# Kernel tuning notes

Measured on AMD Instinct MI355X. Metric: run time of the kernel, lower is better.

The kernel has to match this reference:

```python
import jax, jax.numpy as jnp
import numpy as np

B, S, D, Fd, M, H, L = 4, 1024, 1024, 4096, 512, 16, 2
HD = D // H
EPS = 1e-5


def _ln(x, s, b):
    m = jnp.mean(x, axis=-1, keepdims=True)
    v = jnp.mean((x - m) ** 2, axis=-1, keepdims=True)
    return (x - m) * jax.lax.rsqrt(v + EPS) * s + b


def _mha(x, Wq, bq, Wk, bk, Wv, bv, Wo, bo):
    b_, s_, _ = x.shape
    Q = (x @ Wq + bq).reshape(b_, s_, H, HD)
    K = (x @ Wk + bk).reshape(b_, s_, H, HD)
    V = (x @ Wv + bv).reshape(b_, s_, H, HD)
    scores = jnp.einsum('bihd,bjhd->bhij', Q, K) / np.sqrt(HD).astype(np.float32)
    w = jax.nn.softmax(scores, axis=-1)
    out = jnp.einsum('bhij,bjhd->bihd', w, V).reshape(b_, s_, D)
    return out @ Wo + bo


def setup_inputs() -> dict:
    key = jax.random.key(0)
    ks = iter(jax.random.split(key, 40))
    w = lambda shape: jax.random.normal(next(ks), shape, jnp.float32) * 0.02
    inp = {
        'x': jax.random.normal(next(ks), (B, S, D), jnp.float32),
        # stacked per-global-layer params [L, ...]
        'Wq': w((L, D, D)), 'bq': jnp.zeros((L, D)),
        'Wk': w((L, D, D)), 'bk': jnp.zeros((L, D)),
        'Wv': w((L, D, D)), 'bv': jnp.zeros((L, D)),
        'Wo': w((L, D, D)), 'bo': jnp.zeros((L, D)),
        'W1': w((L, D, Fd)), 'b1': jnp.zeros((L, Fd)),
        'W2': w((L, Fd, D)), 'b2': jnp.zeros((L, D)),
        'n1s': jnp.ones((L, D)), 'n1b': jnp.zeros((L, D)),
        'n2s': jnp.ones((L, D)), 'n2b': jnp.zeros((L, D)),
        # top-level params
        'ln1s': jnp.ones((D,)), 'ln1b': jnp.zeros((D,)),
        'ln2s': jnp.ones((D,)), 'ln2b': jnp.zeros((D,)),
        'ln3s': jnp.ones((D,)), 'ln3b': jnp.zeros((D,)),
        'Wb': w((D, M)), 'bb': jnp.zeros((M,)),      # backbone stand-in
        'Wm': w((M, D)), 'bm': jnp.zeros((D,)),      # self.linear
        'Wf1': w((D, Fd)), 'bf1': jnp.zeros((Fd,)),  # top feed_forward
        'Wf2': w((Fd, D)), 'bf2': jnp.zeros((D,)),
    }
    return inp


def reference(x, Wq, bq, Wk, bk, Wv, bv, Wo, bo, W1, b1, W2, b2,
              n1s, n1b, n2s, n2b, ln1s, ln1b, ln2s, ln2b, ln3s, ln3b,
              Wb, bb, Wm, bm, Wf1, bf1, Wf2, bf2):
    # dropout is identity (eval mode)
    # global branch: stacked EncoderLayers
    g = x
    for i in range(L):
        a = _mha(g, Wq[i], bq[i], Wk[i], bk[i], Wv[i], bv[i], Wo[i], bo[i])
        g = _ln(g + a, n1s[i], n1b[i])
        ff = jax.nn.relu(g @ W1[i] + b1[i]) @ W2[i] + b2[i]
        g = _ln(g + ff, n2s[i], n2b[i])

    def local(frac):
        st = S // frac
        xs = x[:, -st:, :]
        mo = (xs @ Wb + bb) @ Wm + bm
        y = _ln(xs + mo, ln1s, ln1b)
        return jnp.pad(y, ((0, 0), (S - st, 0), (0, 0)))

    output = g + local(2) + local(4)  # S >= 4 branch
    h = _ln(output + x, ln2s, ln2b)
    ff = jax.nn.relu(output @ Wf1 + bf1) @ Wf2 + bf2
    return _ln(h + ff, ln3s, ln3b)
```

## Files before the change

### kernel.cpp

```cpp
#include <hip/hip_runtime.h>
#include <stdint.h>


typedef short   s16x8 __attribute__((ext_vector_type(8)));
typedef float   f32x4 __attribute__((ext_vector_type(4)));
typedef uint16_t u16x8 __attribute__((ext_vector_type(8)));
typedef uint16_t u16x4 __attribute__((ext_vector_type(4)));

__device__ __forceinline__ float bf2f(uint16_t h) {
    union { uint32_t u; float f; } c; c.u = ((uint32_t)h) << 16; return c.f;
}
__device__ __forceinline__ uint16_t f2bf(float f) {
    union { float f; uint32_t u; } c; c.f = f;
    uint32_t u = c.u;
    u += 0x7fffu + ((u >> 16) & 1u);
    return (uint16_t)(u >> 16);
}
__device__ __forceinline__ uint32_t cvt_pk_bf16(float lo, float hi) {
    uint32_t r;
    asm("v_cvt_pk_bf16_f32 %0, %1, %2" : "=v"(r) : "v"(lo), "v"(hi));
    return r;
}

__device__ __forceinline__ void g2l16(const uint16_t* g, uint16_t* l) {
    __builtin_amdgcn_global_load_lds(
        (const __attribute__((address_space(1))) void*)g,
        (__attribute__((address_space(3))) void*)l, 16, 0, 0);
}

template<int MODE>
__global__ __launch_bounds__(256, 2) void gemm128n(
    const uint16_t* __restrict__ A, const uint16_t* __restrict__ Bt,
    const float* __restrict__ bias0, const float* __restrict__ bias1,
    const float* __restrict__ bias2,
    uint16_t* __restrict__ C0, uint16_t* __restrict__ C1,
    uint16_t* __restrict__ C2,
    int N)
{
    __shared__ __align__(16) uint16_t smem[36864];
    uint16_t* sA = smem;
    uint16_t* sB = smem + 12288;

    const int t    = threadIdx.x;
    const int w    = t >> 6;
    const int lane = t & 63;
    const int qd   = lane >> 4;
    const int cc   = lane & 15;
    const int wn   = w * 64;

    const int id  = blockIdx.x;
    const int loc = id >> 3;
    const int bm  = (id & 7) * 4 + (loc & 3);
    const int bn  = loc >> 2;
    const int m0  = bm * 128;
    const int n0  = bn * 256;

    const float* bp = bias0;
    int n0c = n0;
    if (MODE == 3) {
        int seg = n0 >> 10;
        n0c = n0 & 1023;
        bp = (seg == 0) ? bias0 : (seg == 1) ? bias1 : bias2;
    }
    float bb[4];
#pragma unroll
    for (int j = 0; j < 4; ++j) bb[j] = bp[n0c + wn + j * 16 + cc];

    int offA[8], offB[4];
#pragma unroll
    for (int i = 0; i < 8; ++i) {
        int ml = i * 16 + cc;
        offA[i] = ml * 32 + ((qd ^ ((ml >> 1) & 3)) * 8);
    }
#pragma unroll
    for (int j = 0; j < 4; ++j) {
        int nl = wn + j * 16 + cc;
        offB[j] = nl * 32 + ((qd ^ ((nl >> 1) & 3)) * 8);
    }

    const uint16_t* pA[2]; int ldA[2];
#pragma unroll
    for (int is = 0; is < 2; ++is) {
        int gc = is * 256 + t;
        int row = gc >> 2, ph = gc & 3;
        pA[is]  = A + (size_t)(m0 + row) * 1024 + (ph ^ ((row >> 1) & 3)) * 8;
        ldA[is] = (is * 256 + w * 64) * 8;
    }
    const uint16_t* pB[4]; int ldB[4];
#pragma unroll
    for (int is = 0; is < 4; ++is) {
        int gc = is * 256 + t;
        int row = gc >> 2, ph = gc & 3;
        pB[is]  = Bt + (size_t)(n0 + row) * 1024 + (ph ^ ((row >> 1) & 3)) * 8;
        ldB[is] = (is * 256 + w * 64) * 8;
    }
    auto stage = [&](int tt, int slot) {
        int kt = tt * 32;
        uint16_t* dA = sA + slot * 4096;
        uint16_t* dB = sB + slot * 8192;
#pragma unroll
        for (int is = 0; is < 2; ++is) g2l16(pA[is] + kt, dA + ldA[is]);
#pragma unroll
        for (int is = 0; is < 4; ++is) g2l16(pB[is] + kt, dB + ldB[is]);
    };

    f32x4 acc[8][4];
#pragma unroll
    for (int i = 0; i < 8; ++i)
#pragma unroll
        for (int j = 0; j < 4; ++j) acc[i][j] = (f32x4)0.0f;

    stage(0, 0); stage(1, 1);
    asm volatile("s_waitcnt vmcnt(6)" ::: "memory");
    __builtin_amdgcn_s_barrier();

    int cur = 0, pf = 2;
#pragma unroll 1
    for (int kt = 0; kt < 32; ++kt) {
        const uint16_t* sa = sA + cur * 4096;
        const uint16_t* sb = sB + cur * 8192;
        s16x8 av[8], bv[4];
#pragma unroll
        for (int j = 0; j < 4; ++j) bv[j] = *(const s16x8*)(sb + offB[j]);
#pragma unroll
        for (int i = 0; i < 8; ++i) av[i] = *(const s16x8*)(sa + offA[i]);
        if (kt < 30) stage(kt + 2, pf);
        asm volatile("s_waitcnt lgkmcnt(0)" ::: "memory");
        __builtin_amdgcn_sched_barrier(0);
        __builtin_amdgcn_s_setprio(1);
#pragma unroll
        for (int i = 0; i < 8; ++i)
#pragma unroll
            for (int j = 0; j < 4; ++j)
                acc[i][j] = __builtin_amdgcn_mfma_f32_16x16x32_bf16(
                    av[i], bv[j], acc[i][j], 0, 0, 0);
        __builtin_amdgcn_s_setprio(0);
        if (kt < 30)       { asm volatile("s_waitcnt vmcnt(6)" ::: "memory"); }
        else if (kt == 30) { asm volatile("s_waitcnt vmcnt(0)" ::: "memory"); }
        __builtin_amdgcn_s_barrier();
        pf = cur;
        cur = (cur == 2) ? 0 : cur + 1;
    }

    if (MODE == 3 && (n0 >> 10) == 2) {
#pragma unroll
        for (int j = 0; j < 4; ++j) {
            int c = n0c + wn + j * 16 + cc;
            int hh = c >> 6, d = c & 63;
#pragma unroll
            for (int i = 0; i < 8; ++i) {
                int rb = m0 + i * 16 + qd * 4;
                int b = rb >> 10, s = rb & 1023;
                u16x4 o;
#pragma unroll
                for (int r = 0; r < 4; ++r) o[r] = f2bf(acc[i][j][r] + bb[j]);
                *(u16x4*)(C2 + ((size_t)((b * 16 + hh) * 64 + d)) * 1024 + s) = o;
            }
        }
        return;
    }
    {
        uint16_t* C = C0;
        int Nc = N;
        if (MODE == 3) {
            int seg = n0 >> 10;
            C = (seg == 0) ? C0 : C1;
            Nc = 1024;
        }
        constexpr int ST = 264;
#pragma unroll
        for (int i = 0; i < 8; ++i)
#pragma unroll
            for (int j = 0; j < 4; ++j) {
                f32x4 v = acc[i][j];
#pragma unroll
                for (int r = 0; r < 4; ++r) {
                    float val = v[r] + bb[j];
                    if (MODE == 1) val = fmaxf(val, 0.0f);
                    smem[(i * 16 + qd * 4 + r) * ST + wn + j * 16 + cc] = f2bf(val);
                }
            }
        __syncthreads();
#pragma unroll
        for (int p = 0; p < 16; ++p) {
            int row  = p * 8 + (t >> 5);
            int colc = (t & 31) * 8;
            u16x8 v = *(const u16x8*)(smem + row * ST + colc);
            *(u16x8*)(C + (size_t)(m0 + row) * Nc + n0c + colc) = v;
        }
    }
}

template<int MODE, int BN, int BK, int DB>
__global__ __launch_bounds__(256) void gemm_bt(
    const uint16_t* __restrict__ A, const uint16_t* __restrict__ Bt,
    const float* __restrict__ bias0, const float* __restrict__ bias1,
    const float* __restrict__ bias2,
    uint16_t* __restrict__ C0, uint16_t* __restrict__ C1,
    uint16_t* __restrict__ C2,
    int M, int N, int K)
{
    constexpr int JN   = BN / 32;
    constexpr int KS   = BK / 32;
    constexpr int CPR  = BK / 8;
    constexpr int LG   = (BK == 32) ? 2 : 3;
    constexpr int RA   = (128 * BK / 8) / 256;
    constexpr int RB   = (BN  * BK / 8) / 256;
    constexpr int NBUF = DB ? 2 : 1;
    constexpr int STG  = NBUF * (128 + BN) * BK;
    constexpr int EPI  = (MODE == 3) ? 0 : 128 * (BN + 8);
    constexpr int SMEM = (STG > EPI) ? STG : EPI;
    __shared__ __align__(16) uint16_t smem[SMEM];
    uint16_t* sAp = smem;
    uint16_t* sBp = smem + NBUF * 128 * BK;

    const int t    = threadIdx.x;
    const int w    = t >> 6;
    const int lane = t & 63;
    const int qd   = lane >> 4;
    const int cc   = lane & 15;

    int bm, bn;
    {
        int gx = gridDim.x, gy = gridDim.y;
        if ((gy & 7) == 0) {
            int id   = blockIdx.y * gx + blockIdx.x;
            int gpg  = gy >> 3;
            int rest = id >> 3;
            bm = (id & 7) * gpg + rest % gpg;
            bn = rest / gpg;
        } else { bm = blockIdx.y; bn = blockIdx.x; }
    }
    const int m0 = bm * 128;
    const int n0 = bn * BN;
    const int wm = (w >> 1) * 64;
    const int wn = (w & 1) * (BN / 2);

    auto key = [](int row) -> int {
        return (BK == 32) ? ((row >> 1) & 3) : (row & 7);
    };

    f32x4 acc[4][JN];
#pragma unroll
    for (int i = 0; i < 4; ++i)
#pragma unroll
        for (int j = 0; j < JN; ++j) acc[i][j] = (f32x4)0.0f;

    int rA[RA], kA[RA];
#pragma unroll
    for (int is = 0; is < RA; ++is) {
        int gc = is * 256 + t;
        int row = gc >> LG, ph = gc & (CPR - 1);
        rA[is] = row;
        kA[is] = (ph ^ key(row)) * 8;
    }
    int rB[RB], kB[RB];
#pragma unroll
    for (int is = 0; is < RB; ++is) {
        int gc = is * 256 + t;
        int row = gc >> LG, ph = gc & (CPR - 1);
        rB[is] = row;
        kB[is] = (ph ^ key(row)) * 8;
    }
    int offA[4][KS], offB[JN][KS];
#pragma unroll
    for (int i = 0; i < 4; ++i) {
        int ml = wm + i * 16 + cc;
#pragma unroll
        for (int ks = 0; ks < KS; ++ks)
            offA[i][ks] = ml * BK + ((ks * 4 + qd) ^ key(ml)) * 8;
    }
#pragma unroll
    for (int j = 0; j < JN; ++j) {
        int nl = wn + j * 16 + cc;
#pragma unroll
        for (int ks = 0; ks < KS; ++ks)
            offB[j][ks] = nl * BK + ((ks * 4 + qd) ^ key(nl)) * 8;
    }

    auto stage = [&](int kt, int buf) {
#pragma unroll
        for (int is = 0; is < RA; ++is)
            g2l16(A + (size_t)(m0 + rA[is]) * K + kt + kA[is],
                  sAp + (size_t)buf * 128 * BK + (size_t)(is * 256 + w * 64) * 8);
#pragma unroll
        for (int is = 0; is < RB; ++is)
            g2l16(Bt + (size_t)(n0 + rB[is]) * K + kt + kB[is],
                  sBp + (size_t)buf * BN * BK + (size_t)(is * 256 + w * 64) * 8);
    };
    auto compute = [&](int buf) {
        const uint16_t* sa = sAp + (size_t)buf * 128 * BK;
        const uint16_t* sb = sBp + (size_t)buf * BN * BK;
#pragma unroll
        for (int ks = 0; ks < KS; ++ks) {
            s16x8 af[4], bv[JN];
#pragma unroll
            for (int i = 0; i < 4; ++i) af[i] = *(const s16x8*)(sa + offA[i][ks]);
#pragma unroll
            for (int j = 0; j < JN; ++j) bv[j] = *(const s16x8*)(sb + offB[j][ks]);
#pragma unroll
            for (int i = 0; i < 4; ++i)
#pragma unroll
                for (int j = 0; j < JN; ++j)
                    acc[i][j] = __builtin_amdgcn_mfma_f32_16x16x32_bf16(
                        af[i], bv[j], acc[i][j], 0, 0, 0);
        }
    };

    if (DB) {
        stage(0, 0);
        __syncthreads();
        int cur = 0;
        for (int kt = 0; kt < K; kt += BK) {
            if (kt + BK < K) stage(kt + BK, cur ^ 1);
            compute(cur);
            __syncthreads();
            cur ^= 1;
        }
    } else {
        for (int kt = 0; kt < K; kt += BK) {
            stage(kt, 0);
            __syncthreads();
            compute(0);
            __syncthreads();
        }
    }

    if (MODE == 3) {
#pragma unroll
        for (int j = 0; j < JN; ++j) {
            int col = n0 + wn + j * 16 + cc;
            int seg = col >> 10;
            const float* bp = (seg == 0) ? bias0 : (seg == 1) ? bias1 : bias2;
            float bb = bp[col & 1023];
#pragma unroll
            for (int i = 0; i < 4; ++i) {
                f32x4 v = acc[i][j];
#pragma unroll
                for (int r = 0; r < 4; ++r) {
                    float val = v[r] + bb;
                    int row = m0 + wm + i * 16 + qd * 4 + r;
                    if (col < 1024) {
                        C0[(size_t)row * 1024 + col] = f2bf(val);
                    } else if (col < 2048) {
                        C1[(size_t)row * 1024 + (col - 1024)] = f2bf(val);
                    } else {
                        int c = col - 2048;
                        int b = row >> 10, s = row & 1023;
                        int hh = c >> 6, d = c & 63;
                        C2[((size_t)(b * 16 + hh) * 64 + d) * 1024 + s] = f2bf(val);
                    }
                }
            }
        }
    } else {
        constexpr int ST = BN + 8;
#pragma unroll
        for (int j = 0; j < JN; ++j) {
            int col = wn + j * 16 + cc;
            float bb = bias0[n0 + col];
#pragma unroll
            for (int i = 0; i < 4; ++i) {
                f32x4 v = acc[i][j];
#pragma unroll
                for (int r = 0; r < 4; ++r) {
                    float val = v[r] + bb;
                    if (MODE == 1) val = fmaxf(val, 0.0f);
                    smem[(wm + i * 16 + qd * 4 + r) * ST + col] = f2bf(val);
                }
            }
        }
        __syncthreads();
        constexpr int NP  = 128 * BN / 2048;
        constexpr int TPR = BN / 8;
#pragma unroll
        for (int p = 0; p < NP; ++p) {
            int row  = p * (256 / TPR) + t / TPR;
            int colc = (t % TPR) * 8;
            u16x8 v = *(const u16x8*)(smem + row * ST + colc);
            *(u16x8*)(C0 + (size_t)(m0 + row) * N + n0 + colc) = v;
        }
    }
}

#define FA_P 76
__global__ __launch_bounds__(256) void flash_attn(
    const uint16_t* __restrict__ Q, const uint16_t* __restrict__ K,
    const uint16_t* __restrict__ Vt, uint16_t* __restrict__ O)
{
    __shared__ __align__(16) uint16_t QPs[64 * FA_P];
    __shared__ __align__(16) uint16_t Ks[64 * FA_P];
    __shared__ __align__(16) uint16_t Vs[64 * FA_P];

    const int t    = threadIdx.x;
    const int w    = t >> 6;
    const int lane = t & 63;
    const int qd   = lane >> 4;
    const int cc   = lane & 15;
    const int id   = blockIdx.x;
    const int xg   = id & 7;
    const int loc  = id >> 3;
    const int bh   = xg * 8 + (loc >> 4);
    const int qblk = loc & 15;
    const int b    = bh >> 4, hh = bh & 15;
    const size_t rowbase = (size_t)b * 1024;

    int rr[2], ch8[2], lws[2];
    const uint16_t* Kp[2];
    const uint16_t* Vp[2];
#pragma unroll
    for (int is = 0; is < 2; ++is) {
        int c   = is * 256 + t;
        rr[is]  = c >> 3;
        ch8[is] = (c & 7) * 8;
        lws[is] = rr[is] * FA_P + ch8[is];
        Kp[is]  = K  + (rowbase + rr[is]) * 1024 + hh * 64 + ch8[is];
        Vp[is]  = Vt + ((size_t)(bh * 64 + rr[is])) * 1024 + ch8[is];
    }

    u16x8 kr[2], vr[2];
#pragma unroll
    for (int is = 0; is < 2; ++is) {
        kr[is] = *(const u16x8*)(Kp[is]);
        vr[is] = *(const u16x8*)(Vp[is]);
    }

#pragma unroll
    for (int is = 0; is < 2; ++is)
        *(u16x8*)(QPs + lws[is]) =
            *(const u16x8*)(Q + (rowbase + qblk * 64 + rr[is]) * 1024 + hh * 64 + ch8[is]);
    __syncthreads();
    s16x8 aq0 = *(const s16x8*)(QPs + (w * 16 + cc) * FA_P + qd * 8);
    s16x8 aq1 = *(const s16x8*)(QPs + (w * 16 + cc) * FA_P + 32 + qd * 8);
    __syncthreads();

    f32x4 o[4];
    float lrow[4] = {0.0f, 0.0f, 0.0f, 0.0f};
#pragma unroll
    for (int j = 0; j < 4; ++j) o[j] = (f32x4)0.0f;

#pragma unroll 1
    for (int kb = 64; kb <= 1024; kb += 64) {
#pragma unroll
        for (int is = 0; is < 2; ++is) {
            *(u16x8*)(Ks + lws[is]) = kr[is];
            *(u16x8*)(Vs + lws[is]) = vr[is];
        }
        if (kb < 1024) {
#pragma unroll
            for (int is = 0; is < 2; ++is) {
                kr[is] = *(const u16x8*)(Kp[is] + (size_t)kb * 1024);
                vr[is] = *(const u16x8*)(Vp[is] + kb);
            }
        }
        __syncthreads();

        f32x4 sc[4];
#pragma unroll
        for (int j = 0; j < 4; ++j) {
            s16x8 b0 = *(const s16x8*)(Ks + (j * 16 + cc) * FA_P + qd * 8);
            s16x8 b1 = *(const s16x8*)(Ks + (j * 16 + cc) * FA_P + 32 + qd * 8);
            sc[j] = __builtin_amdgcn_mfma_f32_16x16x32_bf16(aq0, b0, (f32x4)0.0f, 0, 0, 0);
            sc[j] = __builtin_amdgcn_mfma_f32_16x16x32_bf16(aq1, b1, sc[j], 0, 0, 0);
        }

#pragma unroll
        for (int r = 0; r < 4; ++r) {
            float p0 = __expf(sc[0][r] * 0.125f);
            float p1 = __expf(sc[1][r] * 0.125f);
            float p2 = __expf(sc[2][r] * 0.125f);
            float p3 = __expf(sc[3][r] * 0.125f);
            lrow[r] += (p0 + p1) + (p2 + p3);
            int prow = (w * 16 + qd * 4 + r) * FA_P + cc;
            uint32_t pk01 = cvt_pk_bf16(p0, p1);
            uint32_t pk23 = cvt_pk_bf16(p2, p3);
            QPs[prow]      = (uint16_t)pk01;
            QPs[prow + 16] = (uint16_t)(pk01 >> 16);
            QPs[prow + 32] = (uint16_t)pk23;
            QPs[prow + 48] = (uint16_t)(pk23 >> 16);
        }

#pragma unroll
        for (int ks = 0; ks < 2; ++ks) {
            s16x8 ap = *(const s16x8*)(QPs + (w * 16 + cc) * FA_P + ks * 32 + qd * 8);
#pragma unroll
            for (int j = 0; j < 4; ++j) {
                s16x8 bv = *(const s16x8*)(Vs + (j * 16 + cc) * FA_P + ks * 32 + qd * 8);
                o[j] = __builtin_amdgcn_mfma_f32_16x16x32_bf16(ap, bv, o[j], 0, 0, 0);
            }
        }
        __syncthreads();
    }

#pragma unroll
    for (int r = 0; r < 4; ++r) {
        float rs = lrow[r];
        rs += __shfl_xor(rs, 1);
        rs += __shfl_xor(rs, 2);
        rs += __shfl_xor(rs, 4);
        rs += __shfl_xor(rs, 8);
        float inv = 1.0f / rs;
        size_t grow = rowbase + qblk * 64 + w * 16 + qd * 4 + r;
#pragma unroll
        for (int j = 0; j < 4; ++j)
            O[grow * 1024 + hh * 64 + j * 16 + cc] = f2bf(o[j][r] * inv);
    }
}

template<int BT, int F32OUT>
__global__ __launch_bounds__(256) void ln_res(
    const uint16_t* __restrict__ A, const void* __restrict__ Bp,
    const float* __restrict__ S, const float* __restrict__ Bi,
    void* __restrict__ outp)
{
    const int row = blockIdx.x, t = threadIdx.x;
    const int w = t >> 6, lane = t & 63;
    u16x4 a4 = *(const u16x4*)(A + (size_t)row * 1024 + t * 4);
    float bvals[4];
    if (BT == 0) {
        u16x4 b4 = *(const u16x4*)((const uint16_t*)Bp + (size_t)row * 1024 + t * 4);
#pragma unroll
        for (int e = 0; e < 4; ++e) bvals[e] = bf2f(b4[e]);
    } else {
        float4 b4 = *(const float4*)((const float*)Bp + (size_t)row * 1024 + t * 4);
        bvals[0] = b4.x; bvals[1] = b4.y; bvals[2] = b4.z; bvals[3] = b4.w;
    }
    float v[4], sum = 0.0f, sq = 0.0f;
#pragma unroll
    for (int e = 0; e < 4; ++e) {
        v[e] = bf2f(a4[e]) + bvals[e];
        sum += v[e];
        sq  += v[e] * v[e];
    }
#pragma unroll
    for (int d = 1; d < 64; d <<= 1) {
        sum += __shfl_xor(sum, d);
        sq  += __shfl_xor(sq, d);
    }
    __shared__ float rs[4], rq[4];
    if (lane == 0) { rs[w] = sum; rq[w] = sq; }
    __syncthreads();
    sum = rs[0] + rs[1] + rs[2] + rs[3];
    sq  = rq[0] + rq[1] + rq[2] + rq[3];
    float mean = sum * (1.0f / 1024.0f);
    float var  = sq * (1.0f / 1024.0f) - mean * mean;
    float rstd = rsqrtf(var + 1e-5f);
    float4 s4  = *(const float4*)(S + t * 4);
    float4 bi4 = *(const float4*)(Bi + t * 4);
    float r0 = (v[0] - mean) * rstd * s4.x + bi4.x;
    float r1 = (v[1] - mean) * rstd * s4.y + bi4.y;
    float r2 = (v[2] - mean) * rstd * s4.z + bi4.z;
    float r3 = (v[3] - mean) * rstd * s4.w + bi4.w;
    if (F32OUT) {
        *(float4*)((float*)outp + (size_t)row * 1024 + t * 4) =
            make_float4(r0, r1, r2, r3);
    } else {
        u16x4 o4;
        o4[0] = f2bf(r0); o4[1] = f2bf(r1); o4[2] = f2bf(r2); o4[3] = f2bf(r3);
        *(u16x4*)((uint16_t*)outp + (size_t)row * 1024 + t * 4) = o4;
    }
}

__global__ __launch_bounds__(256) void add3(
    const uint16_t* __restrict__ g, const uint16_t* __restrict__ y2,
    const uint16_t* __restrict__ y4, uint16_t* __restrict__ out)
{
    size_t e = ((size_t)blockIdx.x * 256 + threadIdx.x) * 4;
    int row = (int)(e >> 10), col = (int)(e & 1023);
    int b = row >> 10, s = row & 1023;
    u16x4 gv = *(const u16x4*)(g + e);
    float v[4];
#pragma unroll
    for (int k = 0; k < 4; ++k) v[k] = bf2f(gv[k]);
    if (s >= 512) {
        u16x4 a = *(const u16x4*)(y2 + ((size_t)(b * 512 + s - 512)) * 1024 + col);
#pragma unroll
        for (int k = 0; k < 4; ++k) v[k] += bf2f(a[k]);
    }
    if (s >= 768) {
        u16x4 a = *(const u16x4*)(y4 + ((size_t)(b * 256 + s - 768)) * 1024 + col);
#pragma unroll
        for (int k = 0; k < 4; ++k) v[k] += bf2f(a[k]);
    }
    u16x4 o4;
#pragma unroll
    for (int k = 0; k < 4; ++k) o4[k] = f2bf(v[k]);
    *(u16x4*)(out + e) = o4;
}

__global__ __launch_bounds__(256) void copy_rows_f32(
    const float* __restrict__ x, uint16_t* __restrict__ out, int lgst)
{
    size_t e = ((size_t)blockIdx.x * 256 + threadIdx.x) * 4;
    int row = (int)(e >> 10), col = (int)(e & 1023);
    int st = 1 << lgst;
    int b = row >> lgst, s = row & (st - 1);
    float4 a = *(const float4*)(x + ((size_t)(b * 1024 + (1024 - st) + s)) * 1024 + col);
    u16x4 o4;
    o4[0] = f2bf(a.x); o4[1] = f2bf(a.y); o4[2] = f2bf(a.z); o4[3] = f2bf(a.w);
    *(u16x4*)(out + e) = o4;
}

__global__ __launch_bounds__(256) void transpose_k(
    const float* __restrict__ W, uint16_t* __restrict__ Wt, int Kd, int Nd)
{
    __shared__ uint16_t tile[64][68];
    const int t  = threadIdx.x;
    const int n0 = blockIdx.x * 64, k0 = blockIdx.y * 64;
#pragma unroll
    for (int p = 0; p < 4; ++p) {
        int k  = p * 16 + (t >> 4);
        int nn = (t & 15) * 4;
        float4 a = *(const float4*)(W + (size_t)(k0 + k) * Nd + n0 + nn);
        tile[nn + 0][k] = f2bf(a.x);
        tile[nn + 1][k] = f2bf(a.y);
        tile[nn + 2][k] = f2bf(a.z);
        tile[nn + 3][k] = f2bf(a.w);
    }
    __syncthreads();
#pragma unroll
    for (int p = 0; p < 2; ++p) {
        int nn = p * 32 + (t >> 3);
        int kk = (t & 7) * 8;
        u16x8 o = *(const u16x8*)(&tile[nn][kk]);
        *(u16x8*)(Wt + (size_t)(n0 + nn) * Kd + k0 + kk) = o;
    }
}

__global__ __launch_bounds__(256) void cvt(
    const float* __restrict__ src, uint16_t* __restrict__ dst)
{
    size_t i = ((size_t)blockIdx.x * 256 + threadIdx.x) * 8;
    float4 a = *(const float4*)(src + i);
    float4 b = *(const float4*)(src + i + 4);
    u16x8 o;
    o[0] = f2bf(a.x); o[1] = f2bf(a.y); o[2] = f2bf(a.z); o[3] = f2bf(a.w);
    o[4] = f2bf(b.x); o[5] = f2bf(b.y); o[6] = f2bf(b.z); o[7] = f2bf(b.w);
    *(u16x8*)(dst + i) = o;
}

extern "C" void kernel_launch(void* const* d_in, const int* in_sizes, int n_in,
                              void* d_out, int out_size, void* d_ws, size_t ws_size,
                              hipStream_t stream)
{
    const float* x    = (const float*)d_in[0];
    const float* Wq   = (const float*)d_in[1];
    const float* bq   = (const float*)d_in[2];
    const float* Wk   = (const float*)d_in[3];
    const float* bk   = (const float*)d_in[4];
    const float* Wv   = (const float*)d_in[5];
    const float* bv   = (const float*)d_in[6];
    const float* Wo   = (const float*)d_in[7];
    const float* bo   = (const float*)d_in[8];
    const float* W1   = (const float*)d_in[9];
    const float* b1   = (const float*)d_in[10];
    const float* W2   = (const float*)d_in[11];
    const float* b2   = (const float*)d_in[12];
    const float* n1s  = (const float*)d_in[13];
    const float* n1b  = (const float*)d_in[14];
    const float* n2s  = (const float*)d_in[15];
    const float* n2b  = (const float*)d_in[16];
    const float* ln1s = (const float*)d_in[17];
    const float* ln1b = (const float*)d_in[18];
    const float* ln2s = (const float*)d_in[19];
    const float* ln2b = (const float*)d_in[20];
    const float* ln3s = (const float*)d_in[21];
    const float* ln3b = (const float*)d_in[22];
    const float* Wb   = (const float*)d_in[23];
    const float* bb   = (const float*)d_in[24];
    const float* Wm   = (const float*)d_in[25];
    const float* bm   = (const float*)d_in[26];
    const float* Wf1  = (const float*)d_in[27];
    const float* bf1  = (const float*)d_in[28];
    const float* Wf2  = (const float*)d_in[29];
    const float* bf2  = (const float*)d_in[30];

    char* ws = (char*)d_ws;
    const size_t MB = (size_t)1 << 20;
    uint16_t* g    = (uint16_t*)(ws);
    uint16_t* tb   = (uint16_t*)(ws + 8 * MB);
    char*     big  = ws + 16 * MB;
    uint16_t* qb   = (uint16_t*)(big);
    uint16_t* kbuf = (uint16_t*)(big + 8 * MB);
    uint16_t* vtb  = (uint16_t*)(big + 16 * MB);
    uint16_t* ob   = (uint16_t*)(big + 24 * MB);
    uint16_t* ffb  = (uint16_t*)(big);
    uint16_t* xbf  = (uint16_t*)(ws + 48 * MB);
    uint16_t* hb   = (uint16_t*)(ws + 48 * MB);
    uint16_t* wT   = (uint16_t*)(ws + 56 * MB);

    auto T = [&](const float* Wsrc, int Kd, int Nd, uint16_t* dst) {
        transpose_k<<<dim3(Nd / 64, Kd / 64), 256, 0, stream>>>(Wsrc, dst, Kd, Nd);
    };

    cvt<<<2048, 256, 0, stream>>>(x, xbf);

    const uint16_t* gin = xbf;
    for (int i = 0; i < 2; ++i) {
        const size_t wOff = (size_t)i * 1024 * 1024;
        const size_t fOff = (size_t)i * 1024 * 4096;
        T(Wq + wOff, 1024, 1024, wT);
        T(Wk + wOff, 1024, 1024, wT + (size_t)1024 * 1024);
        T(Wv + wOff, 1024, 1024, wT + (size_t)2048 * 1024);
        gemm128n<3><<<384, 256, 0, stream>>>(
            gin, wT, bq + i * 1024, bk + i * 1024, bv + i * 1024,
            qb, kbuf, vtb, 3072);
        flash_attn<<<1024, 256, 0, stream>>>(qb, kbuf, vtb, ob);
        T(Wo + wOff, 1024, 1024, wT);
        gemm_bt<0, 64, 64, 1><<<dim3(16, 32), 256, 0, stream>>>(
            ob, wT, bo + i * 1024, nullptr, nullptr, tb, nullptr, nullptr,
            4096, 1024, 1024);
        ln_res<0, 0><<<4096, 256, 0, stream>>>(gin, tb, n1s + i * 1024, n1b + i * 1024, g);
        T(W1 + fOff, 1024, 4096, wT);
        gemm128n<1><<<512, 256, 0, stream>>>(
            g, wT, b1 + i * 4096, nullptr, nullptr, ffb, nullptr, nullptr, 4096);
        T(W2 + fOff, 4096, 1024, wT);
        gemm_bt<0, 64, 64, 1><<<dim3(16, 32), 256, 0, stream>>>(
            ffb, wT, b2 + i * 1024, nullptr, nullptr, tb, nullptr, nullptr,
            4096, 1024, 4096);
        ln_res<0, 0><<<4096, 256, 0, stream>>>(g, tb, n2s + i * 1024, n2b + i * 1024, g);
        gin = g;
    }

    uint16_t* xsc = (uint16_t*)(big);
    uint16_t* lk  = (uint16_t*)(big + 8 * MB);
    uint16_t* mo  = (uint16_t*)(big + 16 * MB);
    uint16_t* yy  = (uint16_t*)(big + 24 * MB);
    copy_rows_f32<<<2048, 256, 0, stream>>>(x, xsc, 9);
    copy_rows_f32<<<1024, 256, 0, stream>>>(x, xsc + (size_t)2048 * 1024, 8);
    uint16_t* WbT = wT;
    uint16_t* WmT = wT + (size_t)512 * 1024;
    T(Wb, 1024, 512, WbT);
    T(Wm, 512, 1024, WmT);
    gemm_bt<0, 64, 64, 1><<<dim3(8, 24), 256, 0, stream>>>(
        xsc, WbT, bb, nullptr, nullptr, lk, nullptr, nullptr, 3072, 512, 1024);
    gemm_bt<0, 64, 64, 1><<<dim3(16, 24), 256, 0, stream>>>(
        lk, WmT, bm, nullptr, nullptr, mo, nullptr, nullptr, 3072, 1024, 512);
    ln_res<0, 0><<<3072, 256, 0, stream>>>(xsc, mo, ln1s, ln1b, yy);
    uint16_t* y2 = yy;
    uint16_t* y4 = yy + (size_t)2048 * 1024;

    add3<<<4096, 256, 0, stream>>>(g, y2, y4, g);
    ln_res<1, 0><<<4096, 256, 0, stream>>>(g, x, ln2s, ln2b, hb);
    T(Wf1, 1024, 4096, wT);
    gemm128n<1><<<512, 256, 0, stream>>>(
        g, wT, bf1, nullptr, nullptr, ffb, nullptr, nullptr, 4096);
    T(Wf2, 4096, 1024, wT);
    gemm_bt<0, 64, 64, 1><<<dim3(16, 32), 256, 0, stream>>>(
        ffb, wT, bf2, nullptr, nullptr, tb, nullptr, nullptr, 4096, 1024, 4096);
    ln_res<0, 1><<<4096, 256, 0, stream>>>(hb, tb, ln3s, ln3b, d_out);
}
```

Baseline: 764.7 us.

## Triple-buffer gemm_bt pipeline, fuse add3 with LayerNorm, batch QKV transposes

The gemm_bt K-loop moves from double buffering with two syncthreads per tile to a three-slot ring. It prefetches two tiles ahead, uses explicit vmcnt waits and a single s_barrier, and raises wave priority around the MFMA block. The add3 kernel is fused with the following LayerNorm, so the summed activation no longer has to be re-read. The three Q/K/V weight transposes become one launch using blockIdx.z. These changes aim to hide global-load latency and cut launch and memory traffic, at the cost of more LDS per block and hand-tuned waitcnt values that depend on the exact number of in-flight loads per stage.

```diff
diff --git a/kernel.cpp b/kernel.cpp
--- a/kernel.cpp
+++ b/kernel.cpp
@@ -191,8 +191,8 @@
     }
 }
 
-template<int MODE, int BN, int BK, int DB>
-__global__ __launch_bounds__(256) void gemm_bt(
+template<int MODE, int BN, int BK>
+__global__ __launch_bounds__(256, 2) void gemm_bt(
     const uint16_t* __restrict__ A, const uint16_t* __restrict__ Bt,
     const float* __restrict__ bias0, const float* __restrict__ bias1,
     const float* __restrict__ bias2,
@@ -200,19 +200,20 @@
     uint16_t* __restrict__ C2,
     int M, int N, int K)
 {
-    constexpr int JN   = BN / 32;
-    constexpr int KS   = BK / 32;
-    constexpr int CPR  = BK / 8;
-    constexpr int LG   = (BK == 32) ? 2 : 3;
-    constexpr int RA   = (128 * BK / 8) / 256;
-    constexpr int RB   = (BN  * BK / 8) / 256;
-    constexpr int NBUF = DB ? 2 : 1;
-    constexpr int STG  = NBUF * (128 + BN) * BK;
-    constexpr int EPI  = (MODE == 3) ? 0 : 128 * (BN + 8);
-    constexpr int SMEM = (STG > EPI) ? STG : EPI;
+    constexpr int JN    = BN / 32;
+    constexpr int KS    = BK / 32;
+    constexpr int CPR   = BK / 8;
+    constexpr int LG    = (BK == 32) ? 2 : 3;
+    constexpr int RA    = (128 * BK / 8) / 256;
+    constexpr int RB    = (BN  * BK / 8) / 256;
+    constexpr int SLOTA = 128 * BK;
+    constexpr int SLOTB = BN * BK;
+    constexpr int STG   = 3 * (SLOTA + SLOTB);
+    constexpr int EPI   = (MODE == 3) ? 0 : 128 * (BN + 8);
+    constexpr int SMEM  = (STG > EPI) ? STG : EPI;
     __shared__ __align__(16) uint16_t smem[SMEM];
-    uint16_t* sAp = smem;
-    uint16_t* sBp = smem + NBUF * 128 * BK;
+    uint16_t* sA = smem;
+    uint16_t* sB = smem + 3 * SLOTA;
 
     const int t    = threadIdx.x;
     const int w    = t >> 6;
@@ -278,52 +279,53 @@
             offB[j][ks] = nl * BK + ((ks * 4 + qd) ^ key(nl)) * 8;
     }
 
-    auto stage = [&](int kt, int buf) {
+    auto stage = [&](int kt, int slot) {
 #pragma unroll
         for (int is = 0; is < RA; ++is)
             g2l16(A + (size_t)(m0 + rA[is]) * K + kt + kA[is],
-                  sAp + (size_t)buf * 128 * BK + (size_t)(is * 256 + w * 64) * 8);
+                  sA + (size_t)slot * SLOTA + (size_t)(is * 256 + w * 64) * 8);
 #pragma unroll
         for (int is = 0; is < RB; ++is)
             g2l16(Bt + (size_t)(n0 + rB[is]) * K + kt + kB[is],
-                  sBp + (size_t)buf * BN * BK + (size_t)(is * 256 + w * 64) * 8);
+                  sB + (size_t)slot * SLOTB + (size_t)(is * 256 + w * 64) * 8);
     };
-    auto compute = [&](int buf) {
-        const uint16_t* sa = sAp + (size_t)buf * 128 * BK;
-        const uint16_t* sb = sBp + (size_t)buf * BN * BK;
+
+    const int NT = K / BK;
+    stage(0, 0); stage(BK, 1);
+    asm volatile("s_waitcnt vmcnt(6)" ::: "memory");
+    __builtin_amdgcn_s_barrier();
+
+    int cur = 0, pf = 2;
+#pragma unroll 1
+    for (int tt = 0; tt < NT; ++tt) {
+        const uint16_t* sa = sA + cur * SLOTA;
+        const uint16_t* sb = sB + cur * SLOTB;
+        s16x8 af[KS][4], bv[KS][JN];
 #pragma unroll
         for (int ks = 0; ks < KS; ++ks) {
-            s16x8 af[4], bv[JN];
-#pragma unroll
-            for (int i = 0; i < 4; ++i) af[i] = *(const s16x8*)(sa + offA[i][ks]);
-#pragma unroll
-            for (int j = 0; j < JN; ++j) bv[j] = *(const s16x8*)(sb + offB[j][ks]);
+#pragma unroll
+            for (int j = 0; j < JN; ++j) bv[ks][j] = *(const s16x8*)(sb + offB[j][ks]);
+#pragma unroll
+            for (int i = 0; i < 4; ++i)  af[ks][i] = *(const s16x8*)(sa + offA[i][ks]);
+        }
+        if (tt + 2 < NT) stage((tt + 2) * BK, pf);
+        asm volatile("s_waitcnt lgkmcnt(0)" ::: "memory");
+        __builtin_amdgcn_sched_barrier(0);
+        __builtin_amdgcn_s_setprio(1);
+#pragma unroll
+        for (int ks = 0; ks < KS; ++ks)
 #pragma unroll
             for (int i = 0; i < 4; ++i)
 #pragma unroll
                 for (int j = 0; j < JN; ++j)
                     acc[i][j] = __builtin_amdgcn_mfma_f32_16x16x32_bf16(
-                        af[i], bv[j], acc[i][j], 0, 0, 0);
-        }
-    };
-
-    if (DB) {
-        stage(0, 0);
-        __syncthreads();
-        int cur = 0;
-        for (int kt = 0; kt < K; kt += BK) {
-            if (kt + BK < K) stage(kt + BK, cur ^ 1);
-            compute(cur);
-            __syncthreads();
-            cur ^= 1;
-        }
-    } else {
-        for (int kt = 0; kt < K; kt += BK) {
-            stage(kt, 0);
-            __syncthreads();
-            compute(0);
-            __syncthreads();
-        }
+                        af[ks][i], bv[ks][j], acc[i][j], 0, 0, 0);
+        __builtin_amdgcn_s_setprio(0);
+        if (tt + 2 < NT)      { asm volatile("s_waitcnt vmcnt(6)" ::: "memory"); }
+        else if (tt + 2 == NT){ asm volatile("s_waitcnt vmcnt(0)" ::: "memory"); }
+        __builtin_amdgcn_s_barrier();
+        pf = cur;
+        cur = (cur == 2) ? 0 : cur + 1;
     }
 
     if (MODE == 3) {
@@ -561,31 +563,61 @@
     }
 }
 
-__global__ __launch_bounds__(256) void add3(
-    const uint16_t* __restrict__ g, const uint16_t* __restrict__ y2,
-    const uint16_t* __restrict__ y4, uint16_t* __restrict__ out)
-{
-    size_t e = ((size_t)blockIdx.x * 256 + threadIdx.x) * 4;
-    int row = (int)(e >> 10), col = (int)(e & 1023);
-    int b = row >> 10, s = row & 1023;
+__global__ __launch_bounds__(256) void add3_ln(
+    uint16_t* __restrict__ g, const uint16_t* __restrict__ y2,
+    const uint16_t* __restrict__ y4, const float* __restrict__ x,
+    const float* __restrict__ S, const float* __restrict__ Bi,
+    uint16_t* __restrict__ h)
+{
+    const int row = blockIdx.x, t = threadIdx.x;
+    const int w = t >> 6, lane = t & 63;
+    const int b = row >> 10, s = row & 1023;
+    const size_t e = (size_t)row * 1024 + t * 4;
     u16x4 gv = *(const u16x4*)(g + e);
     float v[4];
 #pragma unroll
     for (int k = 0; k < 4; ++k) v[k] = bf2f(gv[k]);
     if (s >= 512) {
-        u16x4 a = *(const u16x4*)(y2 + ((size_t)(b * 512 + s - 512)) * 1024 + col);
+        u16x4 a = *(const u16x4*)(y2 + ((size_t)(b * 512 + s - 512)) * 1024 + t * 4);
 #pragma unroll
         for (int k = 0; k < 4; ++k) v[k] += bf2f(a[k]);
     }
     if (s >= 768) {
-        u16x4 a = *(const u16x4*)(y4 + ((size_t)(b * 256 + s - 768)) * 1024 + col);
+        u16x4 a = *(const u16x4*)(y4 + ((size_t)(b * 256 + s - 768)) * 1024 + t * 4);
 #pragma unroll
         for (int k = 0; k < 4; ++k) v[k] += bf2f(a[k]);
     }
     u16x4 o4;
 #pragma unroll
     for (int k = 0; k < 4; ++k) o4[k] = f2bf(v[k]);
-    *(u16x4*)(out + e) = o4;
+    *(u16x4*)(g + e) = o4;
+
+    float4 xv = *(const float4*)(x + e);
+    float v2[4] = { v[0] + xv.x, v[1] + xv.y, v[2] + xv.z, v[3] + xv.w };
+    float sum = 0.0f, sq = 0.0f;
+#pragma unroll
+    for (int k = 0; k < 4; ++k) { sum += v2[k]; sq += v2[k] * v2[k]; }
+#pragma unroll
+    for (int d = 1; d < 64; d <<= 1) {
+        sum += __shfl_xor(sum, d);
+        sq  += __shfl_xor(sq, d);
+    }
+    __shared__ float rs[4], rq[4];
+    if (lane == 0) { rs[w] = sum; rq[w] = sq; }
+    __syncthreads();
+    sum = rs[0] + rs[1] + rs[2] + rs[3];
+    sq  = rq[0] + rq[1] + rq[2] + rq[3];
+    float mean = sum * (1.0f / 1024.0f);
+    float var  = sq * (1.0f / 1024.0f) - mean * mean;
+    float rstd = rsqrtf(var + 1e-5f);
+    float4 s4  = *(const float4*)(S + t * 4);
+    float4 bi4 = *(const float4*)(Bi + t * 4);
+    u16x4 ho;
+    ho[0] = f2bf((v2[0] - mean) * rstd * s4.x + bi4.x);
+    ho[1] = f2bf((v2[1] - mean) * rstd * s4.y + bi4.y);
+    ho[2] = f2bf((v2[2] - mean) * rstd * s4.z + bi4.z);
+    ho[3] = f2bf((v2[3] - mean) * rstd * s4.w + bi4.w);
+    *(u16x4*)(h + e) = ho;
 }
 
 __global__ __launch_bounds__(256) void copy_rows_f32(
@@ -602,8 +634,12 @@
 }
 
 __global__ __launch_bounds__(256) void transpose_k(
-    const float* __restrict__ W, uint16_t* __restrict__ Wt, int Kd, int Nd)
-{
+    const float* __restrict__ W0, const float* __restrict__ W1,
+    const float* __restrict__ W2, uint16_t* __restrict__ Wt, int Kd, int Nd)
+{
+    const int z = blockIdx.z;
+    const float* W = (z == 0) ? W0 : (z == 1) ? W1 : W2;
+    uint16_t* dst = Wt + (size_t)z * Kd * Nd;
     __shared__ uint16_t tile[64][68];
     const int t  = threadIdx.x;
     const int n0 = blockIdx.x * 64, k0 = blockIdx.y * 64;
@@ -623,7 +659,7 @@
         int nn = p * 32 + (t >> 3);
         int kk = (t & 7) * 8;
         u16x8 o = *(const u16x8*)(&tile[nn][kk]);
-        *(u16x8*)(Wt + (size_t)(n0 + nn) * Kd + k0 + kk) = o;
+        *(u16x8*)(dst + (size_t)(n0 + nn) * Kd + k0 + kk) = o;
     }
 }
 
@@ -690,7 +726,8 @@
     uint16_t* wT   = (uint16_t*)(ws + 56 * MB);
 
     auto T = [&](const float* Wsrc, int Kd, int Nd, uint16_t* dst) {
-        transpose_k<<<dim3(Nd / 64, Kd / 64), 256, 0, stream>>>(Wsrc, dst, Kd, Nd);
+        transpose_k<<<dim3(Nd / 64, Kd / 64, 1), 256, 0, stream>>>(
+            Wsrc, Wsrc, Wsrc, dst, Kd, Nd);
     };
 
     cvt<<<2048, 256, 0, stream>>>(x, xbf);
@@ -699,15 +736,14 @@
     for (int i = 0; i < 2; ++i) {
         const size_t wOff = (size_t)i * 1024 * 1024;
         const size_t fOff = (size_t)i * 1024 * 4096;
-        T(Wq + wOff, 1024, 1024, wT);
-        T(Wk + wOff, 1024, 1024, wT + (size_t)1024 * 1024);
-        T(Wv + wOff, 1024, 1024, wT + (size_t)2048 * 1024);
+        transpose_k<<<dim3(16, 16, 3), 256, 0, stream>>>(
+            Wq + wOff, Wk + wOff, Wv + wOff, wT, 1024, 1024);
         gemm128n<3><<<384, 256, 0, stream>>>(
             gin, wT, bq + i * 1024, bk + i * 1024, bv + i * 1024,
             qb, kbuf, vtb, 3072);
         flash_attn<<<1024, 256, 0, stream>>>(qb, kbuf, vtb, ob);
         T(Wo + wOff, 1024, 1024, wT);
-        gemm_bt<0, 64, 64, 1><<<dim3(16, 32), 256, 0, stream>>>(
+        gemm_bt<0, 64, 64><<<dim3(16, 32), 256, 0, stream>>>(
             ob, wT, bo + i * 1024, nullptr, nullptr, tb, nullptr, nullptr,
             4096, 1024, 1024);
         ln_res<0, 0><<<4096, 256, 0, stream>>>(gin, tb, n1s + i * 1024, n1b + i * 1024, g);
@@ -715,7 +751,7 @@
         gemm128n<1><<<512, 256, 0, stream>>>(
             g, wT, b1 + i * 4096, nullptr, nullptr, ffb, nullptr, nullptr, 4096);
         T(W2 + fOff, 4096, 1024, wT);
-        gemm_bt<0, 64, 64, 1><<<dim3(16, 32), 256, 0, stream>>>(
+        gemm_bt<0, 64, 64><<<dim3(16, 32), 256, 0, stream>>>(
             ffb, wT, b2 + i * 1024, nullptr, nullptr, tb, nullptr, nullptr,
             4096, 1024, 4096);
         ln_res<0, 0><<<4096, 256, 0, stream>>>(g, tb, n2s + i * 1024, n2b + i * 1024, g);
@@ -732,21 +768,20 @@
     uint16_t* WmT = wT + (size_t)512 * 1024;
     T(Wb, 1024, 512, WbT);
     T(Wm, 512, 1024, WmT);
-    gemm_bt<0, 64, 64, 1><<<dim3(8, 24), 256, 0, stream>>>(
+    gemm_bt<0, 64, 64><<<dim3(8, 24), 256, 0, stream>>>(
         xsc, WbT, bb, nullptr, nullptr, lk, nullptr, nullptr, 3072, 512, 1024);
-    gemm_bt<0, 64, 64, 1><<<dim3(16, 24), 256, 0, stream>>>(
+    gemm_bt<0, 64, 64><<<dim3(16, 24), 256, 0, stream>>>(
         lk, WmT, bm, nullptr, nullptr, mo, nullptr, nullptr, 3072, 1024, 512);
     ln_res<0, 0><<<3072, 256, 0, stream>>>(xsc, mo, ln1s, ln1b, yy);
     uint16_t* y2 = yy;
     uint16_t* y4 = yy + (size_t)2048 * 1024;
 
-    add3<<<4096, 256, 0, stream>>>(g, y2, y4, g);
-    ln_res<1, 0><<<4096, 256, 0, stream>>>(g, x, ln2s, ln2b, hb);
+    add3_ln<<<4096, 256, 0, stream>>>(g, y2, y4, x, ln2s, ln2b, hb);
     T(Wf1, 1024, 4096, wT);
     gemm128n<1><<<512, 256, 0, stream>>>(
         g, wT, bf1, nullptr, nullptr, ffb, nullptr, nullptr, 4096);
     T(Wf2, 4096, 1024, wT);
-    gemm_bt<0, 64, 64, 1><<<dim3(16, 32), 256, 0, stream>>>(
+    gemm_bt<0, 64, 64><<<dim3(16, 32), 256, 0, stream>>>(
         ffb, wT, bf2, nullptr, nullptr, tb, nullptr, nullptr, 4096, 1024, 4096);
     ln_res<0, 1><<<4096, 256, 0, stream>>>(hb, tb, ln3s, ln3b, d_out);
 }
```

Measured after the change: 720.5 us. 5.8% less time.
